# Optimization experiments

Measured on AMD Instinct MI355X. Metric: run time of the kernel, lower is better.

The kernel has to match this reference:

```python
import jax, jax.numpy as jnp
import numpy as np

B, N, C = 8, 1024, 768
H = 12
D = C // H  # head_dim = 64


def setup_inputs() -> dict:
    key = jax.random.key(0)
    k1, k2, k3 = jax.random.split(key, 3)
    s = 0.02
    x = jax.random.normal(k1, (B, N, C), dtype=jnp.float32)
    w_qkv = jax.random.normal(k2, (C, 3 * C), dtype=jnp.float32) * s
    w_proj = jax.random.normal(k3, (C, C), dtype=jnp.float32) * s
    b_proj = jnp.zeros((C,), dtype=jnp.float32)
    return {"x": x, "w_qkv": w_qkv, "w_proj": w_proj, "b_proj": b_proj}


def reference(x, w_qkv, w_proj, b_proj):
    b, n, c = x.shape
    h, d = H, c // H
    # qkv projection (no bias), split into q,k,v with shape [B,H,N,D]
    qkv = (x @ w_qkv).reshape(b, n, 3, h, d).transpose(2, 0, 3, 1, 4)
    q, k, v = qkv[0], qkv[1], qkv[2]
    scale = d ** -0.5
    # explicit [B,H,N,N] score matrix (module returns attn weights)
    attn = jax.nn.softmax(jnp.einsum('bhid,bhjd->bhij', q, k) * scale, axis=-1)
    # dropout p=0.0 -> identity
    out = jnp.einsum('bhij,bhjd->bhid', attn, v)  # [B,H,N,D]
    out = out.transpose(0, 2, 1, 3).reshape(b, n, c)
    out = out @ w_proj + b_proj
    return out, attn
```

## Files before the change

kernel.cpp:

```cpp
#include <hip/hip_runtime.h>
#include <stdint.h>

constexpr int B = 8, N = 1024, C = 768, H = 12, D = 64;
constexpr int M = B * N;
constexpr int NQKV = 3 * C;
constexpr float SCALE = 0.125f;

typedef _Float16 f16;
typedef _Float16 f16x8 __attribute__((ext_vector_type(8)));
typedef _Float16 f16x4 __attribute__((ext_vector_type(4)));
typedef float    f32x4 __attribute__((ext_vector_type(4)));

__device__ __forceinline__ void gl_lds16(const void* g, void* lds_base) {
    auto gp = (const __attribute__((address_space(1))) uint32_t*)(uintptr_t)g;
    auto lp = (__attribute__((address_space(3))) uint32_t*)(uint32_t)(uintptr_t)lds_base;
    __builtin_amdgcn_global_load_lds(gp, lp, 16, 0, 0);
}

__global__ __launch_bounds__(256)
void conv_x_kernel(const float* __restrict__ x, f16* __restrict__ xh)
{
    size_t i = (size_t)blockIdx.x * 256 + threadIdx.x;
    float4 v = ((const float4*)x)[i];
    f16x4 h = { (f16)v.x, (f16)v.y, (f16)v.z, (f16)v.w };
    *(f16x4*)(xh + 4 * i) = h;
}

__global__ __launch_bounds__(256)
void transpose_conv(const float* __restrict__ src, f16* __restrict__ dst,
                    int rows, int cols)
{
    __shared__ float tile[32][33];
    const int tx = threadIdx.x & 31, ty = threadIdx.x >> 5;
    const int bx = blockIdx.x * 32, by = blockIdx.y * 32;
    #pragma unroll
    for (int i = 0; i < 4; ++i)
        tile[ty + 8 * i][tx] = src[(size_t)(by + ty + 8 * i) * cols + bx + tx];
    __syncthreads();
    #pragma unroll
    for (int i = 0; i < 4; ++i)
        dst[(size_t)(bx + ty + 8 * i) * rows + by + tx] = (f16)tile[tx][ty + 8 * i];
}

__global__ __launch_bounds__(256)
void qkv_gemm_h(const f16* __restrict__ A, const f16* __restrict__ Bt,
                f16* __restrict__ qh, f16* __restrict__ kh, f16* __restrict__ vth)
{
    __shared__ f16 Ah[128 * 32];
    __shared__ f16 Bh[128 * 32];
    const int t = threadIdx.x, w = t >> 6, l = t & 63;
    const int mbase = blockIdx.y * 128, nbase = blockIdx.x * 128;
    const int wm = (w >> 1) * 64, wn = (w & 1) * 64;
    const int fr = l & 15, fq = l >> 4;

    f32x4 acc[4][4];
    #pragma unroll
    for (int i = 0; i < 4; ++i)
        #pragma unroll
        for (int j = 0; j < 4; ++j) acc[i][j] = (f32x4){0.f, 0.f, 0.f, 0.f};

    for (int kb = 0; kb < 768; kb += 32) {
        #pragma unroll
        for (int i = 0; i < 2; ++i) {
            int p = w * 2 + i;
            int r = p * 16 + (l >> 2), c = l & 3;
            gl_lds16(A + (size_t)(mbase + r) * 768 + kb + c * 8, Ah + p * 512);
            gl_lds16(Bt + (size_t)(nbase + r) * 768 + kb + c * 8, Bh + p * 512);
        }
        __syncthreads();
        f16x8 af[4], bf[4];
        #pragma unroll
        for (int mt = 0; mt < 4; ++mt)
            af[mt] = *(const f16x8*)&Ah[(wm + mt * 16 + fr) * 32 + fq * 8];
        #pragma unroll
        for (int nt = 0; nt < 4; ++nt)
            bf[nt] = *(const f16x8*)&Bh[(wn + nt * 16 + fr) * 32 + fq * 8];
        #pragma unroll
        for (int mt = 0; mt < 4; ++mt)
            #pragma unroll
            for (int nt = 0; nt < 4; ++nt)
                acc[mt][nt] = __builtin_amdgcn_mfma_f32_16x16x32_f16(af[mt], bf[nt], acc[mt][nt], 0, 0, 0);
        __syncthreads();
    }

    const int seg = nbase / 768;
    #pragma unroll
    for (int mt = 0; mt < 4; ++mt) {
        int tok0 = mbase + wm + mt * 16 + fq * 4;
        int bb = tok0 >> 10, nn0 = tok0 & 1023;
        #pragma unroll
        for (int nt = 0; nt < 4; ++nt) {
            int od = nbase + wn + nt * 16 + fr;
            int rem = od - seg * 768;
            int hh = rem >> 6, dd = rem & 63;
            if (seg == 2) {
                f16x4 pv = { (f16)acc[mt][nt][0], (f16)acc[mt][nt][1],
                             (f16)acc[mt][nt][2], (f16)acc[mt][nt][3] };
                *(f16x4*)(vth + ((size_t)(bb * H + hh) * 64 + dd) * 1024 + nn0) = pv;
            } else {
                f16* dst = (seg == 0) ? qh : kh;
                size_t base = (size_t)(bb * H + hh) * 1024;
                #pragma unroll
                for (int rg = 0; rg < 4; ++rg)
                    dst[(base + nn0 + rg) * 64 + dd] = (f16)acc[mt][nt][rg];
            }
        }
    }
}

__global__ __launch_bounds__(256)
void attn_fused(const f16* __restrict__ qh, const f16* __restrict__ kh,
                const f16* __restrict__ vth, float* __restrict__ attn,
                f16* __restrict__ ctxh)
{
    __shared__ f16 sQ[16 * 72];
    __shared__ f16 sKV[128 * 64];
    __shared__ f16 sPh[16 * 1032];
    __shared__ float sRed[2][4][16];

    const int t = threadIdx.x, w = t >> 6, l = t & 63;
    const int bh = blockIdx.x >> 6, qt = blockIdx.x & 63;
    const int row0 = qt * 16;
    const size_t kvbase = (size_t)bh * (1024 * 64);
    const int fr = l & 15, fq = l >> 4;

    {
        int r = t >> 4, d4 = (t & 15) * 4;
        *(f16x4*)&sQ[r * 72 + d4] = *(const f16x4*)(qh + kvbase + (size_t)(row0 + r) * 64 + d4);
    }
    __syncthreads();

    f16x8 af[2];
    #pragma unroll
    for (int ks = 0; ks < 2; ++ks)
        af[ks] = *(const f16x8*)&sQ[fr * 72 + ks * 32 + fq * 8];

    f32x4 sacc[8][2];
    #pragma unroll
    for (int jc = 0; jc < 8; ++jc) {
        sacc[jc][0] = (f32x4){0.f, 0.f, 0.f, 0.f};
        sacc[jc][1] = (f32x4){0.f, 0.f, 0.f, 0.f};
    }

    for (int jc = 0; jc < 8; ++jc) {
        #pragma unroll
        for (int i = 0; i < 4; ++i) {
            int p = w * 4 + i;
            int r = p * 8 + (l >> 3);
            int c = (l & 7) ^ (r & 7);
            gl_lds16(kh + kvbase + (size_t)(jc * 128 + r) * 64 + c * 8, sKV + p * 512);
        }
        __syncthreads();
        #pragma unroll
        for (int nt2 = 0; nt2 < 2; ++nt2) {
            int brow = w * 32 + nt2 * 16 + fr;
            #pragma unroll
            for (int ks = 0; ks < 2; ++ks) {
                int cc = (ks * 4 + fq) ^ (brow & 7);
                f16x8 bf = *(const f16x8*)&sKV[brow * 64 + cc * 8];
                sacc[jc][nt2] = __builtin_amdgcn_mfma_f32_16x16x32_f16(af[ks], bf, sacc[jc][nt2], 0, 0, 0);
            }
        }
        __syncthreads();
    }

    float mrow[4] = {-1e30f, -1e30f, -1e30f, -1e30f};
    #pragma unroll
    for (int jc = 0; jc < 8; ++jc)
        #pragma unroll
        for (int nt2 = 0; nt2 < 2; ++nt2)
            #pragma unroll
            for (int r = 0; r < 4; ++r)
                mrow[r] = fmaxf(mrow[r], sacc[jc][nt2][r]);
    #pragma unroll
    for (int off = 1; off < 16; off <<= 1)
        #pragma unroll
        for (int r = 0; r < 4; ++r)
            mrow[r] = fmaxf(mrow[r], __shfl_xor(mrow[r], off));
    if (fr == 0)
        #pragma unroll
        for (int r = 0; r < 4; ++r) sRed[0][w][fq * 4 + r] = mrow[r];
    __syncthreads();

    float Mv[4];
    #pragma unroll
    for (int r = 0; r < 4; ++r) {
        int row = fq * 4 + r;
        float m = fmaxf(fmaxf(sRed[0][0][row], sRed[0][1][row]),
                        fmaxf(sRed[0][2][row], sRed[0][3][row]));
        Mv[r] = m * SCALE;
    }
    float srow[4] = {0.f, 0.f, 0.f, 0.f};
    #pragma unroll
    for (int jc = 0; jc < 8; ++jc)
        #pragma unroll
        for (int nt2 = 0; nt2 < 2; ++nt2)
            #pragma unroll
            for (int r = 0; r < 4; ++r) {
                float p = __expf(sacc[jc][nt2][r] * SCALE - Mv[r]);
                sacc[jc][nt2][r] = p;
                srow[r] += p;
            }
    #pragma unroll
    for (int off = 1; off < 16; off <<= 1)
        #pragma unroll
        for (int r = 0; r < 4; ++r)
            srow[r] += __shfl_xor(srow[r], off);
    if (fr == 0)
        #pragma unroll
        for (int r = 0; r < 4; ++r) sRed[1][w][fq * 4 + r] = srow[r];
    __syncthreads();

    float inv[4];
    #pragma unroll
    for (int r = 0; r < 4; ++r) {
        int row = fq * 4 + r;
        inv[r] = 1.0f / (sRed[1][0][row] + sRed[1][1][row] + sRed[1][2][row] + sRed[1][3][row]);
    }

    float* ab = attn + ((size_t)bh << 20) + (size_t)row0 * 1024;
    #pragma unroll
    for (int jc = 0; jc < 8; ++jc)
        #pragma unroll
        for (int nt2 = 0; nt2 < 2; ++nt2) {
            int col = jc * 128 + w * 32 + nt2 * 16 + fr;
            #pragma unroll
            for (int r = 0; r < 4; ++r) {
                int row = fq * 4 + r;
                float pv = sacc[jc][nt2][r] * inv[r];
                ab[(size_t)row * 1024 + col] = pv;
                sPh[row * 1032 + col] = (f16)pv;
            }
        }
    __syncthreads();

    f32x4 oacc = (f32x4){0.f, 0.f, 0.f, 0.f};
    for (int jc = 0; jc < 8; ++jc) {
        #pragma unroll
        for (int i = 0; i < 4; ++i) {
            int p = w * 4 + i;
            int r = p * 4 + (l >> 4);
            int c = (l & 15) ^ (r & 15);
            gl_lds16(vth + kvbase + (size_t)r * 1024 + jc * 128 + c * 8, sKV + p * 512);
        }
        __syncthreads();
        #pragma unroll
        for (int ks = 0; ks < 4; ++ks) {
            f16x8 pf = *(const f16x8*)&sPh[fr * 1032 + jc * 128 + ks * 32 + fq * 8];
            int brow = w * 16 + fr;
            int cc = (ks * 4 + fq) ^ (brow & 15);
            f16x8 vf = *(const f16x8*)&sKV[brow * 128 + cc * 8];
            oacc = __builtin_amdgcn_mfma_f32_16x16x32_f16(pf, vf, oacc, 0, 0, 0);
        }
        __syncthreads();
    }

    const int bb = bh / H, hh = bh - bb * H;
    int tok0 = bb * 1024 + row0 + fq * 4;
    int cd = hh * 64 + w * 16 + fr;
    #pragma unroll
    for (int rg = 0; rg < 4; ++rg)
        ctxh[(size_t)(tok0 + rg) * 768 + cd] = (f16)oacc[rg];
}

__global__ __launch_bounds__(256)
void proj_gemm_h(const f16* __restrict__ A, const f16* __restrict__ Bt,
                 const float* __restrict__ bias, float* __restrict__ out)
{
    __shared__ f16 Ah[128 * 32];
    __shared__ f16 Bh[128 * 32];
    const int t = threadIdx.x, w = t >> 6, l = t & 63;
    const int mbase = blockIdx.y * 128, nbase = blockIdx.x * 128;
    const int wm = (w >> 1) * 64, wn = (w & 1) * 64;
    const int fr = l & 15, fq = l >> 4;

    f32x4 acc[4][4];
    #pragma unroll
    for (int i = 0; i < 4; ++i)
        #pragma unroll
        for (int j = 0; j < 4; ++j) acc[i][j] = (f32x4){0.f, 0.f, 0.f, 0.f};

    for (int kb = 0; kb < 768; kb += 32) {
        #pragma unroll
        for (int i = 0; i < 2; ++i) {
            int p = w * 2 + i;
            int r = p * 16 + (l >> 2), c = l & 3;
            gl_lds16(A + (size_t)(mbase + r) * 768 + kb + c * 8, Ah + p * 512);
            gl_lds16(Bt + (size_t)(nbase + r) * 768 + kb + c * 8, Bh + p * 512);
        }
        __syncthreads();
        f16x8 af[4], bf[4];
        #pragma unroll
        for (int mt = 0; mt < 4; ++mt)
            af[mt] = *(const f16x8*)&Ah[(wm + mt * 16 + fr) * 32 + fq * 8];
        #pragma unroll
        for (int nt = 0; nt < 4; ++nt)
            bf[nt] = *(const f16x8*)&Bh[(wn + nt * 16 + fr) * 32 + fq * 8];
        #pragma unroll
        for (int mt = 0; mt < 4; ++mt)
            #pragma unroll
            for (int nt = 0; nt < 4; ++nt)
                acc[mt][nt] = __builtin_amdgcn_mfma_f32_16x16x32_f16(af[mt], bf[nt], acc[mt][nt], 0, 0, 0);
        __syncthreads();
    }

    #pragma unroll
    for (int mt = 0; mt < 4; ++mt) {
        int tok0 = mbase + wm + mt * 16 + fq * 4;
        #pragma unroll
        for (int nt = 0; nt < 4; ++nt) {
            int od = nbase + wn + nt * 16 + fr;
            float bv = bias[od];
            #pragma unroll
            for (int rg = 0; rg < 4; ++rg)
                out[(size_t)(tok0 + rg) * 768 + od] = acc[mt][nt][rg] + bv;
        }
    }
}

extern "C" void kernel_launch(void* const* d_in, const int* in_sizes, int n_in,
                              void* d_out, int out_size, void* d_ws, size_t ws_size,
                              hipStream_t stream)
{
    (void)in_sizes; (void)n_in; (void)out_size; (void)ws_size;
    const float* x      = (const float*)d_in[0];
    const float* w_qkv  = (const float*)d_in[1];
    const float* w_proj = (const float*)d_in[2];
    const float* b_proj = (const float*)d_in[3];

    float* out  = (float*)d_out;
    float* attn = out + (size_t)B * N * C;

    const size_t HND = (size_t)B * H * N * D;
    f16* xh     = (f16*)d_ws;
    f16* wqkvT  = xh + HND;
    f16* wprojT = wqkvT + 1769472;
    f16* qh     = wprojT + 589824;
    f16* kh     = qh + HND;
    f16* vth    = kh + HND;
    f16* ctxh   = vth + HND;

    conv_x_kernel<<<dim3(6144), 256, 0, stream>>>(x, xh);
    transpose_conv<<<dim3(NQKV / 32, C / 32), 256, 0, stream>>>(w_qkv, wqkvT, C, NQKV);
    transpose_conv<<<dim3(C / 32, C / 32), 256, 0, stream>>>(w_proj, wprojT, C, C);
    qkv_gemm_h<<<dim3(NQKV / 128, M / 128), 256, 0, stream>>>(xh, wqkvT, qh, kh, vth);
    attn_fused<<<dim3(B * H * (N / 16)), 256, 0, stream>>>(qh, kh, vth, attn, ctxh);
    proj_gemm_h<<<dim3(C / 128, M / 128), 256, 0, stream>>>(ctxh, wprojT, b_proj, out);
}
```

Measured before the change: 663.4 us.

## Double-buffer K/V staging and widen attention blocks to 32 query rows

The attention kernel now processes 32 query rows per 512-thread block, so each K/V tile loaded into LDS is shared by two row groups of warps. K and V tiles are double-buffered, and the next tile's async global-to-LDS load is issued before computing on the current one, with explicit waitcnt and barriers. P is staged per 128-column chunk into a small LDS buffer instead of a full 16x1024 buffer, which cuts LDS use. The fp32 attention matrix write is moved after the PV loop. The cost is hand-managed wait counts and higher register pressure from launch bounds of 512 threads at 4 blocks.

```diff
diff --git a/kernel.cpp b/kernel.cpp
--- a/kernel.cpp
+++ b/kernel.cpp
@@ -10,6 +10,10 @@
 typedef _Float16 f16x8 __attribute__((ext_vector_type(8)));
 typedef _Float16 f16x4 __attribute__((ext_vector_type(4)));
 typedef float    f32x4 __attribute__((ext_vector_type(4)));
+
+#define FENCE() asm volatile("" ::: "memory")
+#define BARRIER() do { FENCE(); __builtin_amdgcn_s_barrier(); FENCE(); } while (0)
+#define WAIT_LGKM0() asm volatile("s_waitcnt lgkmcnt(0)" ::: "memory")
 
 __device__ __forceinline__ void gl_lds16(const void* g, void* lds_base) {
     auto gp = (const __attribute__((address_space(1))) uint32_t*)(uintptr_t)g;
@@ -108,32 +112,55 @@
     }
 }
 
-__global__ __launch_bounds__(256)
+__global__ __launch_bounds__(512, 4)
 void attn_fused(const f16* __restrict__ qh, const f16* __restrict__ kh,
                 const f16* __restrict__ vth, float* __restrict__ attn,
                 f16* __restrict__ ctxh)
 {
-    __shared__ f16 sQ[16 * 72];
-    __shared__ f16 sKV[128 * 64];
-    __shared__ f16 sPh[16 * 1032];
-    __shared__ float sRed[2][4][16];
+    __shared__ f16 sQ[32 * 72];
+    __shared__ f16 sKV[2][8192];
+    __shared__ f16 sP2[2][32 * 136];
+    __shared__ float sRed[2][8][32];
 
     const int t = threadIdx.x, w = t >> 6, l = t & 63;
-    const int bh = blockIdx.x >> 6, qt = blockIdx.x & 63;
-    const int row0 = qt * 16;
+    const int rg = w >> 2, cg = w & 3;
+    const int bh = blockIdx.x >> 5, qt = blockIdx.x & 31;
+    const int row0 = qt * 32;
     const size_t kvbase = (size_t)bh * (1024 * 64);
     const int fr = l & 15, fq = l >> 4;
 
+    auto stageK = [&](int jc, f16* dst) {
+        #pragma unroll
+        for (int i = 0; i < 2; ++i) {
+            int p = w * 2 + i;
+            int r = p * 8 + (l >> 3);
+            int c = (l & 7) ^ (r & 7);
+            gl_lds16(kh + kvbase + (size_t)(jc * 128 + r) * 64 + c * 8, dst + p * 512);
+        }
+    };
+    auto stageV = [&](int jc, f16* dst) {
+        #pragma unroll
+        for (int i = 0; i < 2; ++i) {
+            int p = w * 2 + i;
+            int r = p * 4 + (l >> 4);
+            int c = (l & 15) ^ (r & 15);
+            gl_lds16(vth + kvbase + (size_t)r * 1024 + jc * 128 + c * 8, dst + p * 512);
+        }
+    };
+
     {
         int r = t >> 4, d4 = (t & 15) * 4;
-        *(f16x4*)&sQ[r * 72 + d4] = *(const f16x4*)(qh + kvbase + (size_t)(row0 + r) * 64 + d4);
-    }
-    __syncthreads();
+        f16x4 qv = *(const f16x4*)(qh + kvbase + (size_t)(row0 + r) * 64 + d4);
+        stageK(0, sKV[0]);
+        *(f16x4*)&sQ[r * 72 + d4] = qv;
+    }
+    WAIT_LGKM0();
+    BARRIER();
 
     f16x8 af[2];
     #pragma unroll
     for (int ks = 0; ks < 2; ++ks)
-        af[ks] = *(const f16x8*)&sQ[fr * 72 + ks * 32 + fq * 8];
+        af[ks] = *(const f16x8*)&sQ[(rg * 16 + fr) * 72 + ks * 32 + fq * 8];
 
     f32x4 sacc[8][2];
     #pragma unroll
@@ -142,27 +169,32 @@
         sacc[jc][1] = (f32x4){0.f, 0.f, 0.f, 0.f};
     }
 
+    #pragma unroll
     for (int jc = 0; jc < 8; ++jc) {
-        #pragma unroll
-        for (int i = 0; i < 4; ++i) {
-            int p = w * 4 + i;
-            int r = p * 8 + (l >> 3);
-            int c = (l & 7) ^ (r & 7);
-            gl_lds16(kh + kvbase + (size_t)(jc * 128 + r) * 64 + c * 8, sKV + p * 512);
-        }
-        __syncthreads();
+        const int cur = jc & 1;
+        if (jc < 7) {
+            stageK(jc + 1, sKV[cur ^ 1]);
+            asm volatile("s_waitcnt vmcnt(2)" ::: "memory");
+        } else {
+            asm volatile("s_waitcnt vmcnt(0)" ::: "memory");
+        }
+        BARRIER();
+        __builtin_amdgcn_sched_barrier(0);
         #pragma unroll
         for (int nt2 = 0; nt2 < 2; ++nt2) {
-            int brow = w * 32 + nt2 * 16 + fr;
+            int brow = cg * 32 + nt2 * 16 + fr;
             #pragma unroll
             for (int ks = 0; ks < 2; ++ks) {
-                int cc = (ks * 4 + fq) ^ (brow & 7);
-                f16x8 bf = *(const f16x8*)&sKV[brow * 64 + cc * 8];
+                int slot = (ks * 4 + fq) ^ (brow & 7);
+                f16x8 bf = *(const f16x8*)&sKV[cur][brow * 64 + slot * 8];
                 sacc[jc][nt2] = __builtin_amdgcn_mfma_f32_16x16x32_f16(af[ks], bf, sacc[jc][nt2], 0, 0, 0);
             }
         }
-        __syncthreads();
-    }
+        WAIT_LGKM0();
+        BARRIER();
+    }
+
+    stageV(0, sKV[0]);
 
     float mrow[4] = {-1e30f, -1e30f, -1e30f, -1e30f};
     #pragma unroll
@@ -179,15 +211,16 @@
             mrow[r] = fmaxf(mrow[r], __shfl_xor(mrow[r], off));
     if (fr == 0)
         #pragma unroll
-        for (int r = 0; r < 4; ++r) sRed[0][w][fq * 4 + r] = mrow[r];
-    __syncthreads();
+        for (int r = 0; r < 4; ++r) sRed[0][w][rg * 16 + fq * 4 + r] = mrow[r];
+    WAIT_LGKM0();
+    BARRIER();
 
     float Mv[4];
     #pragma unroll
     for (int r = 0; r < 4; ++r) {
-        int row = fq * 4 + r;
-        float m = fmaxf(fmaxf(sRed[0][0][row], sRed[0][1][row]),
-                        fmaxf(sRed[0][2][row], sRed[0][3][row]));
+        int row = rg * 16 + fq * 4 + r;
+        float m = fmaxf(fmaxf(sRed[0][rg * 4 + 0][row], sRed[0][rg * 4 + 1][row]),
+                        fmaxf(sRed[0][rg * 4 + 2][row], sRed[0][rg * 4 + 3][row]));
         Mv[r] = m * SCALE;
     }
     float srow[4] = {0.f, 0.f, 0.f, 0.f};
@@ -208,14 +241,46 @@
             srow[r] += __shfl_xor(srow[r], off);
     if (fr == 0)
         #pragma unroll
-        for (int r = 0; r < 4; ++r) sRed[1][w][fq * 4 + r] = srow[r];
-    __syncthreads();
+        for (int r = 0; r < 4; ++r) sRed[1][w][rg * 16 + fq * 4 + r] = srow[r];
+    WAIT_LGKM0();
+    BARRIER();
 
     float inv[4];
     #pragma unroll
     for (int r = 0; r < 4; ++r) {
-        int row = fq * 4 + r;
-        inv[r] = 1.0f / (sRed[1][0][row] + sRed[1][1][row] + sRed[1][2][row] + sRed[1][3][row]);
+        int row = rg * 16 + fq * 4 + r;
+        inv[r] = 1.0f / (sRed[1][rg * 4 + 0][row] + sRed[1][rg * 4 + 1][row] +
+                         sRed[1][rg * 4 + 2][row] + sRed[1][rg * 4 + 3][row]);
+    }
+
+    f32x4 oacc = (f32x4){0.f, 0.f, 0.f, 0.f};
+    #pragma unroll
+    for (int jc = 0; jc < 8; ++jc) {
+        const int cur = jc & 1;
+        if (jc < 7) stageV(jc + 1, sKV[cur ^ 1]);
+        #pragma unroll
+        for (int nt2 = 0; nt2 < 2; ++nt2) {
+            int col = cg * 32 + nt2 * 16 + fr;
+            #pragma unroll
+            for (int r = 0; r < 4; ++r) {
+                int row = rg * 16 + fq * 4 + r;
+                sP2[cur][row * 136 + col] = (f16)(sacc[jc][nt2][r] * inv[r]);
+            }
+        }
+        if (jc < 7) asm volatile("s_waitcnt vmcnt(2) lgkmcnt(0)" ::: "memory");
+        else        asm volatile("s_waitcnt vmcnt(0) lgkmcnt(0)" ::: "memory");
+        BARRIER();
+        __builtin_amdgcn_sched_barrier(0);
+        #pragma unroll
+        for (int ks = 0; ks < 4; ++ks) {
+            f16x8 pf = *(const f16x8*)&sP2[cur][(rg * 16 + fr) * 136 + ks * 32 + fq * 8];
+            int brow = cg * 16 + fr;
+            int slot = (ks * 4 + fq) ^ (brow & 15);
+            f16x8 vf = *(const f16x8*)&sKV[cur][brow * 128 + slot * 8];
+            oacc = __builtin_amdgcn_mfma_f32_16x16x32_f16(pf, vf, oacc, 0, 0, 0);
+        }
+        WAIT_LGKM0();
+        BARRIER();
     }
 
     float* ab = attn + ((size_t)bh << 20) + (size_t)row0 * 1024;
@@ -223,44 +288,20 @@
     for (int jc = 0; jc < 8; ++jc)
         #pragma unroll
         for (int nt2 = 0; nt2 < 2; ++nt2) {
-            int col = jc * 128 + w * 32 + nt2 * 16 + fr;
+            int col = jc * 128 + cg * 32 + nt2 * 16 + fr;
             #pragma unroll
             for (int r = 0; r < 4; ++r) {
-                int row = fq * 4 + r;
-                float pv = sacc[jc][nt2][r] * inv[r];
-                ab[(size_t)row * 1024 + col] = pv;
-                sPh[row * 1032 + col] = (f16)pv;
-            }
-        }
-    __syncthreads();
-
-    f32x4 oacc = (f32x4){0.f, 0.f, 0.f, 0.f};
-    for (int jc = 0; jc < 8; ++jc) {
-        #pragma unroll
-        for (int i = 0; i < 4; ++i) {
-            int p = w * 4 + i;
-            int r = p * 4 + (l >> 4);
-            int c = (l & 15) ^ (r & 15);
-            gl_lds16(vth + kvbase + (size_t)r * 1024 + jc * 128 + c * 8, sKV + p * 512);
-        }
-        __syncthreads();
-        #pragma unroll
-        for (int ks = 0; ks < 4; ++ks) {
-            f16x8 pf = *(const f16x8*)&sPh[fr * 1032 + jc * 128 + ks * 32 + fq * 8];
-            int brow = w * 16 + fr;
-            int cc = (ks * 4 + fq) ^ (brow & 15);
-            f16x8 vf = *(const f16x8*)&sKV[brow * 128 + cc * 8];
-            oacc = __builtin_amdgcn_mfma_f32_16x16x32_f16(pf, vf, oacc, 0, 0, 0);
-        }
-        __syncthreads();
-    }
+                int row = rg * 16 + fq * 4 + r;
+                ab[(size_t)row * 1024 + col] = sacc[jc][nt2][r] * inv[r];
+            }
+        }
 
     const int bb = bh / H, hh = bh - bb * H;
-    int tok0 = bb * 1024 + row0 + fq * 4;
-    int cd = hh * 64 + w * 16 + fr;
-    #pragma unroll
-    for (int rg = 0; rg < 4; ++rg)
-        ctxh[(size_t)(tok0 + rg) * 768 + cd] = (f16)oacc[rg];
+    int tok0 = bb * 1024 + row0 + rg * 16 + fq * 4;
+    int cd = hh * 64 + cg * 16 + fr;
+    #pragma unroll
+    for (int rgi = 0; rgi < 4; ++rgi)
+        ctxh[(size_t)(tok0 + rgi) * 768 + cd] = (f16)oacc[rgi];
 }
 
 __global__ __launch_bounds__(256)
@@ -344,6 +385,6 @@
     transpose_conv<<<dim3(NQKV / 32, C / 32), 256, 0, stream>>>(w_qkv, wqkvT, C, NQKV);
     transpose_conv<<<dim3(C / 32, C / 32), 256, 0, stream>>>(w_proj, wprojT, C, C);
     qkv_gemm_h<<<dim3(NQKV / 128, M / 128), 256, 0, stream>>>(xh, wqkvT, qh, kh, vth);
-    attn_fused<<<dim3(B * H * (N / 16)), 256, 0, stream>>>(qh, kh, vth, attn, ctxh);
+    attn_fused<<<dim3(B * H * (N / 32)), 512, 0, stream>>>(qh, kh, vth, attn, ctxh);
     proj_gemm_h<<<dim3(C / 128, M / 128), 256, 0, stream>>>(ctxh, wprojT, b_proj, out);
 }
```

Measured after the change: 570.8 us. -14.0%, faster.
